# Performance work log

Measured on AMD Instinct MI355X. Metric: run time of the kernel, lower is better.

Reference implementation:

```python
import jax, jax.numpy as jnp
import numpy as np

B, IN, H, O, DEPTH = 16384, 64, 128, 32, 4


def _xavier(k, shape):
    fan_in, fan_out = shape[-2], shape[-1]
    lim = float(np.sqrt(6.0 / (fan_in + fan_out)))
    return jax.random.uniform(k, shape, jnp.float32, -lim, lim)


def _gru(x, h, wi, bi, wh, bh):
    # x: [B,1,O], h: [B,1,H]; wi: [3,O,H], wh: [3,H,H]
    r = jax.nn.sigmoid(x @ wi[0] + bi[0] + h @ wh[0] + bh[0])
    z = jax.nn.sigmoid(x @ wi[1] + bi[1] + h @ wh[1] + bh[1])
    n = jnp.tanh(x @ wi[2] + bi[2] + r * (h @ wh[2] + bh[2]))
    return (1.0 - z) * n + z * h


def setup_inputs() -> dict:
    key = jax.random.key(0)
    ks = jax.random.split(key, 10)
    return {
        "z": jax.random.normal(ks[0], (B, 1, IN), jnp.float32),
        "z2h_w": _xavier(ks[1], (IN, H)), "z2h_b": jnp.zeros((H,), jnp.float32),
        "h2o_w": _xavier(ks[2], (H, O)), "h2o_b": jnp.zeros((O,), jnp.float32),
        "gru_a_wi": _xavier(ks[3], (3, O, H)), "gru_a_bi": jnp.zeros((3, H), jnp.float32),
        "gru_a_wh": _xavier(ks[4], (3, H, H)), "gru_a_bh": jnp.zeros((3, H), jnp.float32),
        "gru_f_wi": _xavier(ks[5], (3, O, H)), "gru_f_bi": jnp.zeros((3, H), jnp.float32),
        "gru_f_wh": _xavier(ks[6], (3, H, H)), "gru_f_bh": jnp.zeros((3, H), jnp.float32),
        "u_a_w": _xavier(ks[7], (H, H)), "u_a_b": jnp.zeros((H,), jnp.float32),
        "u_f_w": _xavier(ks[8], (H, H)), "u_f_b": jnp.zeros((H,), jnp.float32),
        "depth": DEPTH,
    }


def reference(z, z2h_w, z2h_b, h2o_w, h2o_b,
              gru_a_wi, gru_a_bi, gru_a_wh, gru_a_bh,
              gru_f_wi, gru_f_bi, gru_f_wh, gru_f_bh,
              u_a_w, u_a_b, u_f_w, u_f_b, depth):
    preds = []

    def node(h_a, d):
        # h_a: [B,1,H] incoming (ancestral) hidden for this node
        pred = h_a @ h2o_w + h2o_b            # [B,1,O] symbol logits
        probs = jax.nn.softmax(pred, axis=2)
        preds.append(pred)
        h_ai = _gru(probs, h_a, gru_a_wi, gru_a_bi, gru_a_wh, gru_a_bh)
        if d > 0:
            # first child: gets ancestral hidden directly
            probs_f = node(h_ai, d - 1)
            # second child: fraternal GRU over first child's root probs,
            # combined with this node's incoming hidden via u_f / u_a
            h_f = _gru(probs_f, h_ai, gru_f_wi, gru_f_bi, gru_f_wh, gru_f_bh)
            h2 = jnp.tanh(h_f @ u_f_w + u_f_b + h_a @ u_a_w + u_a_b)
            node(h2, d - 1)
        return probs

    hidden = z @ z2h_w + z2h_b                # [B,1,H]
    node(hidden, int(depth))
    return jnp.stack(preds, axis=0)           # [n_nodes, B, 1, O] preorder
```

## Files before the change

### kernel.cpp

```cpp
#include <hip/hip_runtime.h>
#include <cstddef>


#define BB   16384
#define HH   128
#define OO   32
#define ROWS 64

typedef __attribute__((ext_vector_type(8))) short bf8;
typedef __attribute__((ext_vector_type(4))) float f4;

#define MFMA(a, b, c) __builtin_amdgcn_mfma_f32_16x16x32_bf16(a, b, c, 0, 0, 0)

#define PW_Z2H 0
#define PW_AWI 8192
#define PW_AWH 20480
#define PW_FWI 69632
#define PW_FWH 81920
#define PW_UA  131072
#define PW_UF  147456
#define PW_H2O 163840
#define PW_END 167936

#define SH   136
#define PSLD 40

#define BA_RZ  0
#define BA_BH2 256
#define BA_BI2 384
#define BF_RZ  512
#define BF_BH2 768
#define BF_BI2 896
#define BU     1024
#define BZ2H   1152
#define BH2O   1280
#define BIAS_N 1312

__device__ __forceinline__ short f2bf(float f) {
  union { float f; unsigned u; } v; v.f = f;
  unsigned r = v.u + 0x7fff + ((v.u >> 16) & 1);
  return (short)(r >> 16);
}
__device__ __forceinline__ float bf2f(short h) {
  union { unsigned u; float f; } v;
  v.u = ((unsigned)(unsigned short)h) << 16;
  return v.f;
}
__device__ __forceinline__ float rcp_(float x) { return __builtin_amdgcn_rcpf(x); }
__device__ __forceinline__ float sigmoidf_(float x) { return rcp_(1.0f + __expf(-x)); }
__device__ __forceinline__ float tanhf_(float x) {
  float ax = fabsf(x), e = __expf(-2.0f * ax);
  float t = (1.0f - e) * rcp_(1.0f + e);
  return x >= 0.0f ? t : -t;
}

template <int K, int N>
__device__ __forceinline__ void repack_one(const float* __restrict__ W,
                                           short* __restrict__ P, int idx) {
  const int KC = K / 32;
  const int j = idx & 7, lane = (idx >> 3) & 63, rest = idx >> 9;
  const int kc = rest % KC, nt = rest / KC;
  const int k = kc * 32 + ((lane >> 4) << 3) + j;
  const int n = nt * 16 + (lane & 15);
  P[idx] = f2bf(W[(size_t)k * N + n]);
}

__global__ __launch_bounds__(256) void k_repack(
    const float* __restrict__ z2hw, const float* __restrict__ awi,
    const float* __restrict__ awh, const float* __restrict__ fwi,
    const float* __restrict__ fwh, const float* __restrict__ uaw,
    const float* __restrict__ ufw, const float* __restrict__ h2ow,
    short* __restrict__ ws) {
  const int t = blockIdx.x * 256 + threadIdx.x;
  if (t < PW_AWI)        repack_one<64, 128>(z2hw, ws + PW_Z2H, t - PW_Z2H);
  else if (t < PW_AWH)   repack_one<96, 128>(awi, ws + PW_AWI, t - PW_AWI);
  else if (t < PW_FWI)   repack_one<384, 128>(awh, ws + PW_AWH, t - PW_AWH);
  else if (t < PW_FWH)   repack_one<96, 128>(fwi, ws + PW_FWI, t - PW_FWI);
  else if (t < PW_UA)    repack_one<384, 128>(fwh, ws + PW_FWH, t - PW_FWH);
  else if (t < PW_UF)    repack_one<128, 128>(uaw, ws + PW_UA, t - PW_UA);
  else if (t < PW_H2O)   repack_one<128, 128>(ufw, ws + PW_UF, t - PW_UF);
  else if (t < PW_END)   repack_one<128, 32>(h2ow, ws + PW_H2O, t - PW_H2O);
}

__device__ __forceinline__ void store_slice(const f4* hv, short* dst, int lane, int w) {
  const int l15 = lane & 15, q = lane >> 4;
#pragma unroll
  for (int rt = 0; rt < 4; ++rt)
#pragma unroll
    for (int j = 0; j < 4; ++j)
      dst[(rt * 16 + q * 4 + j) * SH + w * 16 + l15] = f2bf(hv[rt][j]);
}

__device__ __forceinline__ void gru_slice(const short* xs, const short* hsrc,
                                          const short* wiP, const short* whP,
                                          const float* brz, const float* bh2v,
                                          const float* bi2v,
                                          int lane, int w, f4* hv) {
  const int l15 = lane & 15, q = lane >> 4;
  const int col = w * 16 + l15;
  bf8 ax[4], ah[4][4];
#pragma unroll
  for (int rt = 0; rt < 4; ++rt) {
    ax[rt] = *(const bf8*)(xs + (rt * 16 + l15) * PSLD + q * 8);
#pragma unroll
    for (int c = 0; c < 4; ++c)
      ah[rt][c] = *(const bf8*)(hsrc + (rt * 16 + l15) * SH + c * 32 + q * 8);
  }
  const bf8* wi = (const bf8*)wiP;
  const bf8* wh = (const bf8*)whP;
  f4 t2[4], rg[4];
  {
    const float b = bh2v[col];
#pragma unroll
    for (int rt = 0; rt < 4; ++rt) t2[rt] = (f4){b, b, b, b};
  }
  {
    bf8 W[4];
#pragma unroll
    for (int c = 0; c < 4; ++c) W[c] = wh[(w * 12 + 8 + c) * 64 + lane];
#pragma unroll
    for (int c = 0; c < 4; ++c)
#pragma unroll
      for (int rt = 0; rt < 4; ++rt) t2[rt] = MFMA(ah[rt][c], W[c], t2[rt]);
  }
  {
    const float b = brz[col];
#pragma unroll
    for (int rt = 0; rt < 4; ++rt) rg[rt] = (f4){b, b, b, b};
  }
  {
    bf8 Wx = wi[(w * 3 + 0) * 64 + lane];
    bf8 W[4];
#pragma unroll
    for (int c = 0; c < 4; ++c) W[c] = wh[(w * 12 + 0 + c) * 64 + lane];
#pragma unroll
    for (int rt = 0; rt < 4; ++rt) rg[rt] = MFMA(ax[rt], Wx, rg[rt]);
#pragma unroll
    for (int c = 0; c < 4; ++c)
#pragma unroll
      for (int rt = 0; rt < 4; ++rt) rg[rt] = MFMA(ah[rt][c], W[c], rg[rt]);
  }
#pragma unroll
  for (int k = 0; k < 4; ++k)
#pragma unroll
    for (int j = 0; j < 4; ++j) t2[k][j] *= sigmoidf_(rg[k][j]);
  {
    const float b = bi2v[col];
#pragma unroll
    for (int k = 0; k < 4; ++k)
#pragma unroll
      for (int j = 0; j < 4; ++j) t2[k][j] += b;
  }
  {
    bf8 Wx = wi[(w * 3 + 2) * 64 + lane];
#pragma unroll
    for (int rt = 0; rt < 4; ++rt) t2[rt] = MFMA(ax[rt], Wx, t2[rt]);
  }
  {
    const float b = brz[128 + col];
#pragma unroll
    for (int rt = 0; rt < 4; ++rt) rg[rt] = (f4){b, b, b, b};
  }
  {
    bf8 Wx = wi[(w * 3 + 1) * 64 + lane];
    bf8 W[4];
#pragma unroll
    for (int c = 0; c < 4; ++c) W[c] = wh[(w * 12 + 4 + c) * 64 + lane];
#pragma unroll
    for (int rt = 0; rt < 4; ++rt) rg[rt] = MFMA(ax[rt], Wx, rg[rt]);
#pragma unroll
    for (int c = 0; c < 4; ++c)
#pragma unroll
      for (int rt = 0; rt < 4; ++rt) rg[rt] = MFMA(ah[rt][c], W[c], rg[rt]);
  }
#pragma unroll
  for (int rt = 0; rt < 4; ++rt)
#pragma unroll
    for (int j = 0; j < 4; ++j) {
      const float hc = bf2f(hsrc[(rt * 16 + q * 4 + j) * SH + col]);
      const float zz = sigmoidf_(rg[rt][j]);
      const float nn = tanhf_(t2[rt][j]);
      hv[rt][j] = nn + zz * (hc - nn);
    }
}

__device__ __forceinline__ void pred_node16(const short* hsrc,
                                            const short* h2oP,
                                            const float* bo,
                                            float* spred, short* pdst,
                                            int lane, int w) {
  const int l15 = lane & 15, q = lane >> 4;
  bf8 a[4];
#pragma unroll
  for (int c = 0; c < 4; ++c)
    a[c] = *(const bf8*)(hsrc + (w * 16 + l15) * SH + c * 32 + q * 8);
  const bf8* bw = (const bf8*)h2oP;
  bf8 W[8];
#pragma unroll
  for (int f = 0; f < 8; ++f) W[f] = bw[f * 64 + lane];
  f4 p[2];
#pragma unroll
  for (int nt = 0; nt < 2; ++nt) {
    const float b = bo[nt * 16 + l15];
    f4 acc = (f4){b, b, b, b};
#pragma unroll
    for (int c = 0; c < 4; ++c) acc = MFMA(a[c], W[nt * 4 + c], acc);
    p[nt] = acc;
  }
#pragma unroll
  for (int j = 0; j < 4; ++j) {
    const float v0 = p[0][j], v1 = p[1][j];
    float mx = fmaxf(v0, v1);
#pragma unroll
    for (int s = 1; s < 16; s <<= 1) mx = fmaxf(mx, __shfl_xor(mx, s));
    const float e0 = __expf(v0 - mx), e1 = __expf(v1 - mx);
    float ss = e0 + e1;
#pragma unroll
    for (int s = 1; s < 16; s <<= 1) ss += __shfl_xor(ss, s);
    const float inv = rcp_(ss);
    const int row = w * 16 + q * 4 + j;
    spred[row * 32 + l15] = v0;
    spred[row * 32 + 16 + l15] = v1;
    pdst[row * PSLD + l15] = f2bf(e0 * inv);
    pdst[row * PSLD + 16 + l15] = f2bf(e1 * inv);
  }
}

__device__ const unsigned char d_TYPE[31] =
    {0,1,1,1,1,2,2,1,2,2,1,1,2,2,1,2,2,1,1,1,2,2,1,2,2,1,1,2,2,1,2};
__device__ const unsigned char d_LVL[31] =
    {0,1,2,3,4,4,3,4,4,2,3,4,4,3,4,4,1,2,3,4,4,3,4,4,2,3,4,4,3,4,4};

__global__ __launch_bounds__(512, 2) void k_tree(
    const float* __restrict__ zf, const short* __restrict__ pw,
    const float* __restrict__ z2hb, const float* __restrict__ abi,
    const float* __restrict__ abh, const float* __restrict__ fbi,
    const float* __restrict__ fbh, const float* __restrict__ uab,
    const float* __restrict__ ufb, const float* __restrict__ h2ob,
    float* __restrict__ out) {
  __shared__ __align__(16) short hstk[5 * ROWS * SH];
  __shared__ __align__(16) short hfb[ROWS * SH];
  __shared__ __align__(16) short pstk[5 * ROWS * PSLD];
  __shared__ float bias[BIAS_N];
  float* spred = (float*)hfb;
  const int lane = threadIdx.x & 63;
  const int w = threadIdx.x >> 6;
  const int l15 = lane & 15, q = lane >> 4;
  const int col = w * 16 + l15;
  const int r0 = blockIdx.x * ROWS;

  for (int t = threadIdx.x; t < BIAS_N; t += 512) {
    float v;
    if (t < 256)       v = abi[t] + abh[t];
    else if (t < 384)  v = abh[t];
    else if (t < 512)  v = abi[t - 128];
    else if (t < 768)  v = fbi[t - 512] + fbh[t - 512];
    else if (t < 896)  v = fbh[t - 512];
    else if (t < 1024) v = fbi[t - 640];
    else if (t < 1152) v = uab[t - 1024] + ufb[t - 1024];
    else if (t < 1280) v = z2hb[t - 1152];
    else               v = h2ob[t - 1280];
    bias[t] = v;
  }
  __syncthreads();

  {
    const bf8* wz = (const bf8*)(pw + PW_Z2H);
    const bf8 W0 = wz[(w * 2 + 0) * 64 + lane];
    const bf8 W1 = wz[(w * 2 + 1) * 64 + lane];
    const float b = bias[BZ2H + col];
    f4 hv[4];
#pragma unroll
    for (int rt = 0; rt < 4; ++rt) {
      const float* zr = zf + (size_t)(r0 + rt * 16 + l15) * 64 + q * 8;
      union { short s[8]; bf8 v; } A0, A1;
      {
        const f4 x0 = *(const f4*)zr, x1 = *(const f4*)(zr + 4);
#pragma unroll
        for (int j = 0; j < 4; ++j) { A0.s[j] = f2bf(x0[j]); A0.s[4 + j] = f2bf(x1[j]); }
        const f4 y0 = *(const f4*)(zr + 32), y1 = *(const f4*)(zr + 36);
#pragma unroll
        for (int j = 0; j < 4; ++j) { A1.s[j] = f2bf(y0[j]); A1.s[4 + j] = f2bf(y1[j]); }
      }
      f4 acc = (f4){b, b, b, b};
      acc = MFMA(A0.v, W0, acc);
      acc = MFMA(A1.v, W1, acc);
      hv[rt] = acc;
    }
    store_slice(hv, hstk, lane, w);
  }
  __syncthreads();

#pragma unroll 1
  for (int i = 0; i < 31; ++i) {
    const int t = d_TYPE[i];
    const int L = d_LVL[i];
    short* hcur = hstk + L * ROWS * SH;
    short* pcur = pstk + L * ROWS * PSLD;

    if (t == 2) {
      f4 hf[4];
      gru_slice(pcur, hcur, pw + PW_FWI, pw + PW_FWH,
                bias + BF_RZ, bias + BF_BH2, bias + BF_BI2, lane, w, hf);
      store_slice(hf, hfb, lane, w);
      __syncthreads();
      const short* hpar = hstk + (L - 1) * ROWS * SH;
      const bf8* uf = (const bf8*)(pw + PW_UF);
      const bf8* ua = (const bf8*)(pw + PW_UA);
      bf8 Wf[4], Wa[4];
#pragma unroll
      for (int c = 0; c < 4; ++c) {
        Wf[c] = uf[(w * 4 + c) * 64 + lane];
        Wa[c] = ua[(w * 4 + c) * 64 + lane];
      }
      const float b = bias[BU + col];
      f4 hv[4];
#pragma unroll
      for (int rt = 0; rt < 4; ++rt) {
        f4 acc = (f4){b, b, b, b};
#pragma unroll
        for (int c = 0; c < 4; ++c) {
          const bf8 af = *(const bf8*)(hfb + (rt * 16 + l15) * SH + c * 32 + q * 8);
          const bf8 ap = *(const bf8*)(hpar + (rt * 16 + l15) * SH + c * 32 + q * 8);
          acc = MFMA(af, Wf[c], acc);
          acc = MFMA(ap, Wa[c], acc);
        }
#pragma unroll
        for (int j = 0; j < 4; ++j) acc[j] = tanhf_(acc[j]);
        hv[rt] = acc;
      }
      store_slice(hv, hcur, lane, w);
      __syncthreads();
    }

    if (w < 4)
      pred_node16(hcur, pw + PW_H2O, bias + BH2O, spred, pcur, lane, w);
    __syncthreads();

    {
      const f4 v = *(const f4*)(spred + threadIdx.x * 4);
      __builtin_nontemporal_store(
          v, (f4*)(out + (size_t)i * BB * OO + (size_t)r0 * OO) + threadIdx.x);
    }

    if (L < 4) {
      f4 hv[4];
      gru_slice(pcur, hcur, pw + PW_AWI, pw + PW_AWH,
                bias + BA_RZ, bias + BA_BH2, bias + BA_BI2, lane, w, hv);
      store_slice(hv, hstk + (L + 1) * ROWS * SH, lane, w);
    }
    __syncthreads();
  }
}

extern "C" void kernel_launch(void* const* d_in, const int* in_sizes, int n_in,
                              void* d_out, int out_size, void* d_ws, size_t ws_size,
                              hipStream_t stream) {
  const float* z    = (const float*)d_in[0];
  const float* z2hw = (const float*)d_in[1];
  const float* z2hb = (const float*)d_in[2];
  const float* h2ow = (const float*)d_in[3];
  const float* h2ob = (const float*)d_in[4];
  const float* awi  = (const float*)d_in[5];
  const float* abi  = (const float*)d_in[6];
  const float* awh  = (const float*)d_in[7];
  const float* abh  = (const float*)d_in[8];
  const float* fwi  = (const float*)d_in[9];
  const float* fbi  = (const float*)d_in[10];
  const float* fwh  = (const float*)d_in[11];
  const float* fbh  = (const float*)d_in[12];
  const float* uaw  = (const float*)d_in[13];
  const float* uab  = (const float*)d_in[14];
  const float* ufw  = (const float*)d_in[15];
  const float* ufb  = (const float*)d_in[16];

  float* out = (float*)d_out;
  short* ws  = (short*)d_ws;

  k_repack<<<(PW_END + 255) / 256, 256, 0, stream>>>(
      z2hw, awi, awh, fwi, fwh, uaw, ufw, h2ow, ws);

  k_tree<<<BB / ROWS, 512, 0, stream>>>(
      z, ws, z2hb, abi, abh, fbi, fbh, uab, ufb, h2ob, out);
}
```

Measured before the change: 270.6 us.

## Split GRU into hidden and input parts, overlapping hidden matmuls with prediction

Splits the GRU into a hidden-state part (the h@Wh MFMAs for r, z and n) and an input-plus-epilogue part. The hidden part of the ancestral GRU depends only on the current hidden state, so it now runs before the prediction/softmax step and the barrier, overlapping with the pred work that only 4 of the waves do. It also replaces tanh with a branchless 1-2/(exp(2x)+1) form. The cost is more live accumulator registers across the barrier, which may lower occupancy or cause spills. The new tanh can also overflow exp for large inputs, though it saturates correctly.

```diff
diff --git a/kernel.cpp b/kernel.cpp
--- a/kernel.cpp
+++ b/kernel.cpp
@@ -49,9 +49,8 @@
 __device__ __forceinline__ float rcp_(float x) { return __builtin_amdgcn_rcpf(x); }
 __device__ __forceinline__ float sigmoidf_(float x) { return rcp_(1.0f + __expf(-x)); }
 __device__ __forceinline__ float tanhf_(float x) {
-  float ax = fabsf(x), e = __expf(-2.0f * ax);
-  float t = (1.0f - e) * rcp_(1.0f + e);
-  return x >= 0.0f ? t : -t;
+  const float e = __expf(2.0f * x);
+  return 1.0f - 2.0f * rcp_(e + 1.0f);
 }
 
 template <int K, int N>
@@ -91,94 +90,95 @@
       dst[(rt * 16 + q * 4 + j) * SH + w * 16 + l15] = f2bf(hv[rt][j]);
 }
 
-__device__ __forceinline__ void gru_slice(const short* xs, const short* hsrc,
-                                          const short* wiP, const short* whP,
+__device__ __forceinline__ void gru_hpart(const short* hsrc, const short* whP,
                                           const float* brz, const float* bh2v,
-                                          const float* bi2v,
-                                          int lane, int w, f4* hv) {
+                                          int lane, int w,
+                                          f4* t2, f4* rr, f4* rz) {
   const int l15 = lane & 15, q = lane >> 4;
   const int col = w * 16 + l15;
-  bf8 ax[4], ah[4][4];
-#pragma unroll
-  for (int rt = 0; rt < 4; ++rt) {
-    ax[rt] = *(const bf8*)(xs + (rt * 16 + l15) * PSLD + q * 8);
+  bf8 ah[4][4];
+#pragma unroll
+  for (int rt = 0; rt < 4; ++rt)
 #pragma unroll
     for (int c = 0; c < 4; ++c)
       ah[rt][c] = *(const bf8*)(hsrc + (rt * 16 + l15) * SH + c * 32 + q * 8);
-  }
+  const bf8* wh = (const bf8*)whP;
+  {
+    const float b = bh2v[col];
+#pragma unroll
+    for (int rt = 0; rt < 4; ++rt) t2[rt] = (f4){b, b, b, b};
+  }
+  {
+    const float b = brz[col];
+#pragma unroll
+    for (int rt = 0; rt < 4; ++rt) rr[rt] = (f4){b, b, b, b};
+  }
+  {
+    const float b = brz[128 + col];
+#pragma unroll
+    for (int rt = 0; rt < 4; ++rt) rz[rt] = (f4){b, b, b, b};
+  }
+  {
+    bf8 W[4];
+#pragma unroll
+    for (int c = 0; c < 4; ++c) W[c] = wh[(w * 12 + 8 + c) * 64 + lane];
+#pragma unroll
+    for (int c = 0; c < 4; ++c)
+#pragma unroll
+      for (int rt = 0; rt < 4; ++rt) t2[rt] = MFMA(ah[rt][c], W[c], t2[rt]);
+  }
+  {
+    bf8 W[4];
+#pragma unroll
+    for (int c = 0; c < 4; ++c) W[c] = wh[(w * 12 + 0 + c) * 64 + lane];
+#pragma unroll
+    for (int c = 0; c < 4; ++c)
+#pragma unroll
+      for (int rt = 0; rt < 4; ++rt) rr[rt] = MFMA(ah[rt][c], W[c], rr[rt]);
+  }
+  {
+    bf8 W[4];
+#pragma unroll
+    for (int c = 0; c < 4; ++c) W[c] = wh[(w * 12 + 4 + c) * 64 + lane];
+#pragma unroll
+    for (int c = 0; c < 4; ++c)
+#pragma unroll
+      for (int rt = 0; rt < 4; ++rt) rz[rt] = MFMA(ah[rt][c], W[c], rz[rt]);
+  }
+}
+
+__device__ __forceinline__ void gru_xepi(const short* xs, const short* hsrc,
+                                         const short* wiP, const float* bi2v,
+                                         int lane, int w,
+                                         f4* t2, f4* rr, f4* rz, f4* hv) {
+  const int l15 = lane & 15, q = lane >> 4;
+  const int col = w * 16 + l15;
+  bf8 ax[4];
+#pragma unroll
+  for (int rt = 0; rt < 4; ++rt)
+    ax[rt] = *(const bf8*)(xs + (rt * 16 + l15) * PSLD + q * 8);
   const bf8* wi = (const bf8*)wiP;
-  const bf8* wh = (const bf8*)whP;
-  f4 t2[4], rg[4];
-  {
-    const float b = bh2v[col];
-#pragma unroll
-    for (int rt = 0; rt < 4; ++rt) t2[rt] = (f4){b, b, b, b};
-  }
-  {
-    bf8 W[4];
-#pragma unroll
-    for (int c = 0; c < 4; ++c) W[c] = wh[(w * 12 + 8 + c) * 64 + lane];
-#pragma unroll
-    for (int c = 0; c < 4; ++c)
-#pragma unroll
-      for (int rt = 0; rt < 4; ++rt) t2[rt] = MFMA(ah[rt][c], W[c], t2[rt]);
-  }
-  {
-    const float b = brz[col];
-#pragma unroll
-    for (int rt = 0; rt < 4; ++rt) rg[rt] = (f4){b, b, b, b};
-  }
-  {
-    bf8 Wx = wi[(w * 3 + 0) * 64 + lane];
-    bf8 W[4];
-#pragma unroll
-    for (int c = 0; c < 4; ++c) W[c] = wh[(w * 12 + 0 + c) * 64 + lane];
-#pragma unroll
-    for (int rt = 0; rt < 4; ++rt) rg[rt] = MFMA(ax[rt], Wx, rg[rt]);
-#pragma unroll
-    for (int c = 0; c < 4; ++c)
-#pragma unroll
-      for (int rt = 0; rt < 4; ++rt) rg[rt] = MFMA(ah[rt][c], W[c], rg[rt]);
-  }
-#pragma unroll
-  for (int k = 0; k < 4; ++k)
-#pragma unroll
-    for (int j = 0; j < 4; ++j) t2[k][j] *= sigmoidf_(rg[k][j]);
-  {
-    const float b = bi2v[col];
-#pragma unroll
-    for (int k = 0; k < 4; ++k)
-#pragma unroll
-      for (int j = 0; j < 4; ++j) t2[k][j] += b;
-  }
-  {
-    bf8 Wx = wi[(w * 3 + 2) * 64 + lane];
-#pragma unroll
-    for (int rt = 0; rt < 4; ++rt) t2[rt] = MFMA(ax[rt], Wx, t2[rt]);
-  }
-  {
-    const float b = brz[128 + col];
-#pragma unroll
-    for (int rt = 0; rt < 4; ++rt) rg[rt] = (f4){b, b, b, b};
-  }
-  {
-    bf8 Wx = wi[(w * 3 + 1) * 64 + lane];
-    bf8 W[4];
-#pragma unroll
-    for (int c = 0; c < 4; ++c) W[c] = wh[(w * 12 + 4 + c) * 64 + lane];
-#pragma unroll
-    for (int rt = 0; rt < 4; ++rt) rg[rt] = MFMA(ax[rt], Wx, rg[rt]);
-#pragma unroll
-    for (int c = 0; c < 4; ++c)
-#pragma unroll
-      for (int rt = 0; rt < 4; ++rt) rg[rt] = MFMA(ah[rt][c], W[c], rg[rt]);
-  }
+  const bf8 Wr = wi[(w * 3 + 0) * 64 + lane];
+  const bf8 Wz = wi[(w * 3 + 1) * 64 + lane];
+  const bf8 Wn = wi[(w * 3 + 2) * 64 + lane];
+#pragma unroll
+  for (int rt = 0; rt < 4; ++rt) rr[rt] = MFMA(ax[rt], Wr, rr[rt]);
+  const float b2 = bi2v[col];
+#pragma unroll
+  for (int rt = 0; rt < 4; ++rt)
+#pragma unroll
+    for (int j = 0; j < 4; ++j)
+      t2[rt][j] = t2[rt][j] * sigmoidf_(rr[rt][j]) + b2;
+#pragma unroll
+  for (int rt = 0; rt < 4; ++rt) t2[rt] = MFMA(ax[rt], Wn, t2[rt]);
+#pragma unroll
+  for (int rt = 0; rt < 4; ++rt) rz[rt] = MFMA(ax[rt], Wz, rz[rt]);
 #pragma unroll
   for (int rt = 0; rt < 4; ++rt)
 #pragma unroll
     for (int j = 0; j < 4; ++j) {
       const float hc = bf2f(hsrc[(rt * 16 + q * 4 + j) * SH + col]);
-      const float zz = sigmoidf_(rg[rt][j]);
+      const float zz = sigmoidf_(rz[rt][j]);
       const float nn = tanhf_(t2[rt][j]);
       hv[rt][j] = nn + zz * (hc - nn);
     }
@@ -299,9 +299,11 @@
     short* pcur = pstk + L * ROWS * PSLD;
 
     if (t == 2) {
-      f4 hf[4];
-      gru_slice(pcur, hcur, pw + PW_FWI, pw + PW_FWH,
-                bias + BF_RZ, bias + BF_BH2, bias + BF_BI2, lane, w, hf);
+      f4 ft2[4], frr[4], frz[4], hf[4];
+      gru_hpart(hcur, pw + PW_FWH, bias + BF_RZ, bias + BF_BH2, lane, w,
+                ft2, frr, frz);
+      gru_xepi(pcur, hcur, pw + PW_FWI, bias + BF_BI2, lane, w,
+               ft2, frr, frz, hf);
       store_slice(hf, hfb, lane, w);
       __syncthreads();
       const short* hpar = hstk + (L - 1) * ROWS * SH;
@@ -333,6 +335,10 @@
       __syncthreads();
     }
 
+    f4 t2[4], rr[4], rz[4];
+    if (L < 4)
+      gru_hpart(hcur, pw + PW_AWH, bias + BA_RZ, bias + BA_BH2, lane, w,
+                t2, rr, rz);
     if (w < 4)
       pred_node16(hcur, pw + PW_H2O, bias + BH2O, spred, pcur, lane, w);
     __syncthreads();
@@ -342,11 +348,10 @@
       __builtin_nontemporal_store(
           v, (f4*)(out + (size_t)i * BB * OO + (size_t)r0 * OO) + threadIdx.x);
     }
-
     if (L < 4) {
       f4 hv[4];
-      gru_slice(pcur, hcur, pw + PW_AWI, pw + PW_AWH,
-                bias + BA_RZ, bias + BA_BH2, bias + BA_BI2, lane, w, hv);
+      gru_xepi(pcur, hcur, pw + PW_AWI, bias + BA_BI2, lane, w,
+               t2, rr, rz, hv);
       store_slice(hv, hstk + (L + 1) * ROWS * SH, lane, w);
     }
     __syncthreads();
```

After: 285.7 us. 1.06x slower.

## Overlap GRU hidden matmuls with output head and keep weights in registers

Applied to the files above, without the earlier changes.

Hoists the ancestral GRU's recurrent weights and the h2o weights into registers once per block instead of reloading them at every node. The hidden-state MFMAs of the ancestral GRU now run before the prediction/softmax barrier, so they overlap with the output head, and the x-side MFMAs are applied afterwards. Logits are written straight to global memory rather than staged through shared memory. Softmax drops the max subtraction and tanh uses a simpler formula. Launch bounds are relaxed to one block per SM to make room for the extra registers. The risks are lower occupancy and overflow in exp for large logits, and the final barrier is now skipped at leaf nodes.

```diff
diff --git a/kernel.cpp b/kernel.cpp
--- a/kernel.cpp
+++ b/kernel.cpp
@@ -49,9 +49,8 @@
 __device__ __forceinline__ float rcp_(float x) { return __builtin_amdgcn_rcpf(x); }
 __device__ __forceinline__ float sigmoidf_(float x) { return rcp_(1.0f + __expf(-x)); }
 __device__ __forceinline__ float tanhf_(float x) {
-  float ax = fabsf(x), e = __expf(-2.0f * ax);
-  float t = (1.0f - e) * rcp_(1.0f + e);
-  return x >= 0.0f ? t : -t;
+  const float e = __expf(2.0f * x);
+  return 1.0f - 2.0f * rcp_(e + 1.0f);
 }
 
 template <int K, int N>
@@ -184,54 +183,12 @@
     }
 }
 
-__device__ __forceinline__ void pred_node16(const short* hsrc,
-                                            const short* h2oP,
-                                            const float* bo,
-                                            float* spred, short* pdst,
-                                            int lane, int w) {
-  const int l15 = lane & 15, q = lane >> 4;
-  bf8 a[4];
-#pragma unroll
-  for (int c = 0; c < 4; ++c)
-    a[c] = *(const bf8*)(hsrc + (w * 16 + l15) * SH + c * 32 + q * 8);
-  const bf8* bw = (const bf8*)h2oP;
-  bf8 W[8];
-#pragma unroll
-  for (int f = 0; f < 8; ++f) W[f] = bw[f * 64 + lane];
-  f4 p[2];
-#pragma unroll
-  for (int nt = 0; nt < 2; ++nt) {
-    const float b = bo[nt * 16 + l15];
-    f4 acc = (f4){b, b, b, b};
-#pragma unroll
-    for (int c = 0; c < 4; ++c) acc = MFMA(a[c], W[nt * 4 + c], acc);
-    p[nt] = acc;
-  }
-#pragma unroll
-  for (int j = 0; j < 4; ++j) {
-    const float v0 = p[0][j], v1 = p[1][j];
-    float mx = fmaxf(v0, v1);
-#pragma unroll
-    for (int s = 1; s < 16; s <<= 1) mx = fmaxf(mx, __shfl_xor(mx, s));
-    const float e0 = __expf(v0 - mx), e1 = __expf(v1 - mx);
-    float ss = e0 + e1;
-#pragma unroll
-    for (int s = 1; s < 16; s <<= 1) ss += __shfl_xor(ss, s);
-    const float inv = rcp_(ss);
-    const int row = w * 16 + q * 4 + j;
-    spred[row * 32 + l15] = v0;
-    spred[row * 32 + 16 + l15] = v1;
-    pdst[row * PSLD + l15] = f2bf(e0 * inv);
-    pdst[row * PSLD + 16 + l15] = f2bf(e1 * inv);
-  }
-}
-
 __device__ const unsigned char d_TYPE[31] =
     {0,1,1,1,1,2,2,1,2,2,1,1,2,2,1,2,2,1,1,1,2,2,1,2,2,1,1,2,2,1,2};
 __device__ const unsigned char d_LVL[31] =
     {0,1,2,3,4,4,3,4,4,2,3,4,4,3,4,4,1,2,3,4,4,3,4,4,2,3,4,4,3,4,4};
 
-__global__ __launch_bounds__(512, 2) void k_tree(
+__global__ __launch_bounds__(512, 1) void k_tree(
     const float* __restrict__ zf, const short* __restrict__ pw,
     const float* __restrict__ z2hb, const float* __restrict__ abi,
     const float* __restrict__ abh, const float* __restrict__ fbi,
@@ -242,7 +199,6 @@
   __shared__ __align__(16) short hfb[ROWS * SH];
   __shared__ __align__(16) short pstk[5 * ROWS * PSLD];
   __shared__ float bias[BIAS_N];
-  float* spred = (float*)hfb;
   const int lane = threadIdx.x & 63;
   const int w = threadIdx.x >> 6;
   const int l15 = lane & 15, q = lane >> 4;
@@ -262,6 +218,23 @@
     else               v = h2ob[t - 1280];
     bias[t] = v;
   }
+
+  bf8 waR[4], waZ[4], waN[4];
+  {
+    const bf8* wh = (const bf8*)(pw + PW_AWH);
+#pragma unroll
+    for (int c = 0; c < 4; ++c) {
+      waR[c] = wh[(w * 12 + 0 + c) * 64 + lane];
+      waZ[c] = wh[(w * 12 + 4 + c) * 64 + lane];
+      waN[c] = wh[(w * 12 + 8 + c) * 64 + lane];
+    }
+  }
+  bf8 Wo[8];
+  if (w < 4) {
+    const bf8* bw = (const bf8*)(pw + PW_H2O);
+#pragma unroll
+    for (int f = 0; f < 8; ++f) Wo[f] = bw[f * 64 + lane];
+  }
   __syncthreads();
 
   {
@@ -333,23 +306,104 @@
       __syncthreads();
     }
 
-    if (w < 4)
-      pred_node16(hcur, pw + PW_H2O, bias + BH2O, spred, pcur, lane, w);
+    f4 t2[4], rr[4], rz[4];
+    if (L < 4) {
+      bf8 ah[4][4];
+#pragma unroll
+      for (int rt = 0; rt < 4; ++rt)
+#pragma unroll
+        for (int c = 0; c < 4; ++c)
+          ah[rt][c] = *(const bf8*)(hcur + (rt * 16 + l15) * SH + c * 32 + q * 8);
+      const float bn = bias[BA_BH2 + col];
+      const float br = bias[BA_RZ + col];
+      const float bz = bias[BA_RZ + 128 + col];
+#pragma unroll
+      for (int rt = 0; rt < 4; ++rt) {
+        t2[rt] = (f4){bn, bn, bn, bn};
+        rr[rt] = (f4){br, br, br, br};
+        rz[rt] = (f4){bz, bz, bz, bz};
+      }
+#pragma unroll
+      for (int c = 0; c < 4; ++c)
+#pragma unroll
+        for (int rt = 0; rt < 4; ++rt) t2[rt] = MFMA(ah[rt][c], waN[c], t2[rt]);
+#pragma unroll
+      for (int c = 0; c < 4; ++c)
+#pragma unroll
+        for (int rt = 0; rt < 4; ++rt) rr[rt] = MFMA(ah[rt][c], waR[c], rr[rt]);
+#pragma unroll
+      for (int c = 0; c < 4; ++c)
+#pragma unroll
+        for (int rt = 0; rt < 4; ++rt) rz[rt] = MFMA(ah[rt][c], waZ[c], rz[rt]);
+    }
+    if (w < 4) {
+      bf8 a[4];
+#pragma unroll
+      for (int c = 0; c < 4; ++c)
+        a[c] = *(const bf8*)(hcur + (w * 16 + l15) * SH + c * 32 + q * 8);
+      const float b0 = bias[BH2O + l15];
+      const float b1 = bias[BH2O + 16 + l15];
+      f4 pa = (f4){b0, b0, b0, b0};
+      f4 pb = (f4){b1, b1, b1, b1};
+#pragma unroll
+      for (int c = 0; c < 4; ++c) {
+        pa = MFMA(a[c], Wo[c], pa);
+        pb = MFMA(a[c], Wo[4 + c], pb);
+      }
+      float* ob = out + ((size_t)i * BB + r0 + w * 16 + q * 4) * OO + l15;
+#pragma unroll
+      for (int j = 0; j < 4; ++j) {
+        __builtin_nontemporal_store(pa[j], ob + j * OO);
+        __builtin_nontemporal_store(pb[j], ob + j * OO + 16);
+      }
+#pragma unroll
+      for (int j = 0; j < 4; ++j) {
+        const float e0 = __expf(pa[j]), e1 = __expf(pb[j]);
+        float ss = e0 + e1;
+#pragma unroll
+        for (int s = 1; s < 16; s <<= 1) ss += __shfl_xor(ss, s);
+        const float inv = rcp_(ss);
+        short* pr = pcur + (w * 16 + q * 4 + j) * PSLD;
+        pr[l15] = f2bf(e0 * inv);
+        pr[16 + l15] = f2bf(e1 * inv);
+      }
+    }
     __syncthreads();
 
-    {
-      const f4 v = *(const f4*)(spred + threadIdx.x * 4);
-      __builtin_nontemporal_store(
-          v, (f4*)(out + (size_t)i * BB * OO + (size_t)r0 * OO) + threadIdx.x);
-    }
-
     if (L < 4) {
+      const bf8* wi = (const bf8*)(pw + PW_AWI);
+      const bf8 Wxr = wi[(w * 3 + 0) * 64 + lane];
+      const bf8 Wxz = wi[(w * 3 + 1) * 64 + lane];
+      const bf8 Wxn = wi[(w * 3 + 2) * 64 + lane];
+      bf8 ax[4];
+#pragma unroll
+      for (int rt = 0; rt < 4; ++rt)
+        ax[rt] = *(const bf8*)(pcur + (rt * 16 + l15) * PSLD + q * 8);
+#pragma unroll
+      for (int rt = 0; rt < 4; ++rt) rr[rt] = MFMA(ax[rt], Wxr, rr[rt]);
+      const float b2 = bias[BA_BI2 + col];
+#pragma unroll
+      for (int rt = 0; rt < 4; ++rt)
+#pragma unroll
+        for (int j = 0; j < 4; ++j)
+          t2[rt][j] = t2[rt][j] * sigmoidf_(rr[rt][j]) + b2;
+#pragma unroll
+      for (int rt = 0; rt < 4; ++rt) t2[rt] = MFMA(ax[rt], Wxn, t2[rt]);
+#pragma unroll
+      for (int rt = 0; rt < 4; ++rt) rz[rt] = MFMA(ax[rt], Wxz, rz[rt]);
       f4 hv[4];
-      gru_slice(pcur, hcur, pw + PW_AWI, pw + PW_AWH,
-                bias + BA_RZ, bias + BA_BH2, bias + BA_BI2, lane, w, hv);
+#pragma unroll
+      for (int rt = 0; rt < 4; ++rt)
+#pragma unroll
+        for (int j = 0; j < 4; ++j) {
+          const float hc = bf2f(hcur[(rt * 16 + q * 4 + j) * SH + col]);
+          const float zz = sigmoidf_(rz[rt][j]);
+          const float nn = tanhf_(t2[rt][j]);
+          hv[rt][j] = nn + zz * (hc - nn);
+        }
       store_slice(hv, hstk + (L + 1) * ROWS * SH, lane, w);
-    }
-    __syncthreads();
+      __syncthreads();
+    }
   }
 }
 
```

After: 418.7 us. +54.8%, slower.
